# Kernel tuning notes

Measured on AMD Instinct MI355X. Metric: run time of the kernel, lower is better.

The kernel has to match this reference:

```python
import jax, jax.numpy as jnp
import numpy as np

B, T, L, C = 8, 512, 2048, 256

def setup_inputs() -> dict:
    key = jax.random.key(0)
    ks = jax.random.split(key, 8)
    # center/boundary positions in mel-frame units, a <= b
    e = jax.random.uniform(ks[0], (B, T), jnp.float32) * L
    a = jax.random.uniform(ks[1], (B, T), jnp.float32) * L
    w = jax.random.uniform(ks[2], (B, T), jnp.float32) * 20.0
    b = jnp.minimum(a + w, float(L))
    x_h = jax.random.normal(ks[3], (B, C, T), jnp.float32)
    text_mask = jnp.ones((B, T), dtype=bool)
    mel_mask = jnp.ones((B, L), dtype=jnp.float32)
    sigma = jnp.ones((2,), jnp.float32) * 0.1
    w_hidden = jax.random.normal(ks[4], (2 * C, C), jnp.float32) / np.sqrt(C)
    b_hidden = jnp.zeros((2 * C,), jnp.float32)
    w_out = jax.random.normal(ks[5], (C, 2 * C), jnp.float32) / np.sqrt(2 * C)
    b_out = jnp.zeros((C,), jnp.float32)
    return {"e": e, "a": a, "b": b, "x_h": x_h, "text_mask": text_mask,
            "mel_mask": mel_mask, "sigma": sigma, "w_hidden": w_hidden,
            "b_hidden": b_hidden, "w_out": w_out, "b_out": b_out}

def reference(e, a, b, x_h, text_mask, mel_mask, sigma, w_hidden, b_hidden, w_out, b_out):
    length = mel_mask.shape[-1]
    q = jnp.arange(length, dtype=e.dtype)[None, :] * mel_mask          # [B, L]
    qe = q[:, :, None]                                                 # [B, L, 1]
    energies_e = -((qe - e[:, None, :]) ** 2)                          # [B, L, T]
    energies_boundary = -((jnp.abs(qe - a[:, None, :]) + jnp.abs(qe - b[:, None, :])
                           - (b[:, None, :] - a[:, None, :])) ** 2)    # [B, L, T]
    energies_all = jnp.stack([energies_e, energies_boundary], axis=1)  # [B, 2, L, T]
    real_sigma = jnp.clip(sigma, 1e-6, 3.0)
    energies = energies_all * real_sigma[None, :, None, None]
    energies = jnp.where(text_mask[:, None, None, :], energies, -jnp.inf)
    attns = jax.nn.softmax(energies, axis=-1)                          # [B, 2, L, T]
    # 1x1 conv == channel matmul
    h = jnp.einsum('oc,bct->bot', w_hidden, x_h) + b_hidden[None, :, None]  # [B, 2C, T]
    Bh = h.shape[0]
    h = h.reshape(Bh, 2, C, T).transpose(0, 1, 3, 2)                   # [B, 2, T, C]
    out = jnp.matmul(attns, h)                                         # [B, 2, L, C]
    out = out.transpose(0, 1, 3, 2).reshape(Bh, 2 * C, length)         # [B, 2C, L]
    out = jnp.einsum('oc,bct->bot', w_out, out) + b_out[None, :, None] # [B, C, L]
    return (out, attns, real_sigma)
```

## Files before the change

### kernel.cpp

```cpp
#include <hip/hip_runtime.h>
#include <math.h>

#define B_ 8
#define T_ 512
#define L_ 2048
#define C_ 256

typedef short s16x8 __attribute__((ext_vector_type(8)));
typedef short s16x4 __attribute__((ext_vector_type(4)));
typedef float f32x4 __attribute__((ext_vector_type(4)));

static __device__ __forceinline__ short f2bf(float f) {
  unsigned int u = __float_as_uint(f);
  unsigned int r = u + 0x7FFFu + ((u >> 16) & 1u);
  return (short)(r >> 16);
}

__global__ __launch_bounds__(256) void k_fold(const float* __restrict__ wout,
                                              const float* __restrict__ whid,
                                              const float* __restrict__ bhid,
                                              unsigned short* __restrict__ W2bf,
                                              float* __restrict__ bias2) {
  int blk = blockIdx.x;
  int tid = threadIdx.x;
  if (blk < 512) {
    int s  = blk >> 8;
    int o  = ((blk >> 4) & 15) * 16 + (tid >> 4);
    int c2 = (blk & 15) * 16 + (tid & 15);
    const float* wo = wout + (size_t)o * 512 + s * 256;
    const float* wh = whid + (size_t)(s * 256) * 256 + c2;
    float a0 = 0.f, a1 = 0.f, a2 = 0.f, a3 = 0.f;
    for (int c = 0; c < 256; c += 4) {
      a0 += wo[c]     * wh[(size_t)c * 256];
      a1 += wo[c + 1] * wh[(size_t)(c + 1) * 256];
      a2 += wo[c + 2] * wh[(size_t)(c + 2) * 256];
      a3 += wo[c + 3] * wh[(size_t)(c + 3) * 256];
    }
    W2bf[((size_t)s * 256 + o) * 256 + c2] = (unsigned short)f2bf((a0 + a1) + (a2 + a3));
  } else {
    int s = blk - 512;
    int o = tid;
    const float* wo = wout + (size_t)o * 512 + s * 256;
    const float* bh = bhid + s * 256;
    float ab = 0.f;
    for (int c = 0; c < 256; ++c) ab += wo[c] * bh[c];
    bias2[s * 256 + o] = ab;
  }
}

__global__ __launch_bounds__(256) void k_hp(const float* __restrict__ xh,
                                            const unsigned short* __restrict__ W2bf,
                                            unsigned short* __restrict__ hpB) {
  __shared__ __align__(16) char lds[24576];
  char* As = lds;
  char* Bs = lds + 8192;
  int blk = blockIdx.x;
  int b  = blk >> 5;
  int m0 = ((blk >> 2) & 7) * 64;
  int n0 = (blk & 3) * 128;
  int tid = threadIdx.x;
  int wid = tid >> 6, lane = tid & 63;
  int ln15 = lane & 15, kg = lane >> 4;
  int tg = tid & 31, cg = tid >> 5;

  f32x4 acc[4][2];
#pragma unroll
  for (int mt = 0; mt < 4; ++mt)
#pragma unroll
    for (int nt = 0; nt < 2; ++nt) acc[mt][nt] = {0.f, 0.f, 0.f, 0.f};

  for (int k0 = 0; k0 < 256; k0 += 64) {
#pragma unroll
    for (int it = 0; it < 2; ++it) {
      int gi = it * 256 + tid;
      int r = gi >> 3, j = gi & 7;
      const unsigned short* src = W2bf + (size_t)(m0 + r) * 256 + k0 + ((j ^ (r & 7)) * 8);
      char* dst = As + (size_t)(it * 256 + wid * 64) * 16;
      __builtin_amdgcn_global_load_lds((const __attribute__((address_space(1))) void*)src,
                                       (__attribute__((address_space(3))) void*)dst, 16, 0, 0);
    }
    {
      float4 v[8];
#pragma unroll
      for (int cc = 0; cc < 8; ++cc)
        v[cc] = *(const float4*)&xh[((size_t)b * 256 + k0 + cg * 8 + cc) * 512 + n0 + tg * 4];
#pragma unroll
      for (int tt = 0; tt < 4; ++tt) {
        int trow = tg * 4 + tt;
        s16x8 w = {f2bf(v[0][tt]), f2bf(v[1][tt]), f2bf(v[2][tt]), f2bf(v[3][tt]),
                   f2bf(v[4][tt]), f2bf(v[5][tt]), f2bf(v[6][tt]), f2bf(v[7][tt])};
        *(s16x8*)(Bs + trow * 128 + ((cg ^ (trow & 7)) << 4)) = w;
      }
    }
    __syncthreads();
#pragma unroll
    for (int kk = 0; kk < 2; ++kk) {
      int sl = kk * 4 + kg;
      s16x8 af[4], bfr[2];
#pragma unroll
      for (int mt = 0; mt < 4; ++mt) {
        int r = mt * 16 + ln15;
        af[mt] = *(const s16x8*)(As + r * 128 + ((sl ^ (r & 7)) << 4));
      }
#pragma unroll
      for (int nt = 0; nt < 2; ++nt) {
        int r = wid * 32 + nt * 16 + ln15;
        bfr[nt] = *(const s16x8*)(Bs + r * 128 + ((sl ^ (r & 7)) << 4));
      }
#pragma unroll
      for (int mt = 0; mt < 4; ++mt)
#pragma unroll
        for (int nt = 0; nt < 2; ++nt)
          acc[mt][nt] = __builtin_amdgcn_mfma_f32_16x16x32_bf16(af[mt], bfr[nt], acc[mt][nt], 0, 0, 0);
    }
    __syncthreads();
  }
#pragma unroll
  for (int mt = 0; mt < 4; ++mt)
#pragma unroll
    for (int nt = 0; nt < 2; ++nt) {
      int n = n0 + wid * 32 + nt * 16 + ln15;
#pragma unroll
      for (int e = 0; e < 4; ++e) {
        int m = m0 + mt * 16 + kg * 4 + e;
        hpB[((size_t)b * 512 + m) * 512 + n] = (unsigned short)f2bf(acc[mt][nt][e]);
      }
    }
}

__global__ __launch_bounds__(512) void k_attnout(const float* __restrict__ pe,
                                                 const float* __restrict__ pa,
                                                 const float* __restrict__ pb,
                                                 const float* __restrict__ mel,
                                                 const float* __restrict__ sigma,
                                                 const float* __restrict__ bias2,
                                                 const float* __restrict__ bout,
                                                 const unsigned short* __restrict__ hpB,
                                                 float* __restrict__ outAttn,
                                                 float* __restrict__ outSigma,
                                                 float* __restrict__ out) {
  __shared__ __align__(16) char lds[73728];
  char* Bs0 = lds;
  char* As0 = lds + 65536;
  float* prm  = (float*)lds;
  float* stat = (float*)(lds + 6144);
  float* mval = (float*)(lds + 8192);
  float* idv  = (float*)(lds + 8448);

  int blk = blockIdx.x;
  int b  = blk & 7;
  int l0 = (blk >> 3) << 5;
  int tid = threadIdx.x;
  int wid = tid >> 6, lane = tid & 63;
  int ln15 = lane & 15, kg = lane >> 4;

  prm[tid]        = pe[b * 512 + tid];
  prm[512 + tid]  = pa[b * 512 + tid];
  prm[1024 + tid] = pb[b * 512 + tid];
  float sig0 = fminf(fmaxf(sigma[0], 1e-6f), 3.0f);
  float sig1 = fminf(fmaxf(sigma[1], 1e-6f), 3.0f);
  if (blk == 0 && tid < 2) outSigma[tid] = tid ? sig1 : sig0;
  __syncthreads();

  int pl = tid & 31, grp = tid >> 5;
  int s1 = grp & 1, et = grp >> 1;
  float qv1 = (float)(l0 + pl) * mel[(size_t)b * 2048 + l0 + pl];
  const float4* e4 = (const float4*)(prm + et * 64);
  const float4* a4 = (const float4*)(prm + 512 + et * 64);
  const float4* b4 = (const float4*)(prm + 1024 + et * 64);
  float pm = -INFINITY;
  if (s1 == 0) {
    for (int t4 = 0; t4 < 16; ++t4) {
      float4 ev = e4[t4];
#pragma unroll
      for (int j = 0; j < 4; ++j) {
        float de = qv1 - ev[j];
        pm = fmaxf(pm, -(de * de) * sig0);
      }
    }
  } else {
    for (int t4 = 0; t4 < 16; ++t4) {
      float4 av = a4[t4], bv = b4[t4];
#pragma unroll
      for (int j = 0; j < 4; ++j) {
        float d1 = fabsf(qv1 - av[j]) + fabsf(qv1 - bv[j]) - (bv[j] - av[j]);
        pm = fmaxf(pm, -(d1 * d1) * sig1);
      }
    }
  }
  stat[grp * 32 + pl] = pm;
  __syncthreads();
  if (tid < 64) {
    int s = tid >> 5, l = tid & 31;
    float m = stat[s * 32 + l];
#pragma unroll
    for (int g = 1; g < 8; ++g) m = fmaxf(m, stat[(g * 2 + s) * 32 + l]);
    mval[s * 32 + l] = m;
  }
  __syncthreads();
  float mm = mval[s1 * 32 + pl];
  float psum = 0.f;
  if (s1 == 0) {
    for (int t4 = 0; t4 < 16; ++t4) {
      float4 ev = e4[t4];
#pragma unroll
      for (int j = 0; j < 4; ++j) {
        float de = qv1 - ev[j];
        psum += __expf(fmaf(de * de, -sig0, -mm));
      }
    }
  } else {
    for (int t4 = 0; t4 < 16; ++t4) {
      float4 av = a4[t4], bv = b4[t4];
#pragma unroll
      for (int j = 0; j < 4; ++j) {
        float d1 = fabsf(qv1 - av[j]) + fabsf(qv1 - bv[j]) - (bv[j] - av[j]);
        psum += __expf(fmaf(d1 * d1, -sig1, -mm));
      }
    }
  }
  __syncthreads();
  stat[grp * 32 + pl] = psum;
  __syncthreads();
  if (tid < 64) {
    int s = tid >> 5, l = tid & 31;
    float sum = stat[s * 32 + l];
#pragma unroll
    for (int g = 1; g < 8; ++g) sum += stat[(g * 2 + s) * 32 + l];
    idv[s * 32 + l] = 1.0f / sum;
  }
  __syncthreads();

  {
    int row = tid >> 4, ts16 = tid & 15;
    float qv2 = (float)(l0 + row) * mel[(size_t)b * 2048 + l0 + row];
#pragma unroll
    for (int s = 0; s < 2; ++s) {
      float mm2 = mval[s * 32 + row];
      float iv2 = idv[s * 32 + row];
      float nmm = -mm2;
      float* ap = outAttn + ((size_t)(b * 2 + s) * 2048 + l0 + row) * 512;
#pragma unroll
      for (int j4 = 0; j4 < 8; ++j4) {
        int tb2 = j4 * 64 + ts16 * 4;
        f32x4 v;
        if (s == 0) {
          float4 ev = *(const float4*)(prm + tb2);
#pragma unroll
          for (int j = 0; j < 4; ++j) {
            float de = qv2 - ev[j];
            v[j] = __expf(fmaf(de * de, -sig0, nmm)) * iv2;
          }
        } else {
          float4 av = *(const float4*)(prm + 512 + tb2);
          float4 bv = *(const float4*)(prm + 1024 + tb2);
#pragma unroll
          for (int j = 0; j < 4; ++j) {
            float d1 = fabsf(qv2 - av[j]) + fabsf(qv2 - bv[j]) - (bv[j] - av[j]);
            v[j] = __expf(fmaf(d1 * d1, -sig1, nmm)) * iv2;
          }
        }
        *(f32x4*)(ap + tb2) = v;
      }
    }
  }
  asm volatile("s_waitcnt vmcnt(0)" ::: "memory");
  __builtin_amdgcn_sched_barrier(0);
  __syncthreads();

  int ar = tid >> 4, aj = tid & 15;

  f32x4 acc[2][2];
#pragma unroll
  for (int nt = 0; nt < 2; ++nt) {
    int o = wid * 32 + nt * 16 + ln15;
    float bv = bout[o] + bias2[o] + bias2[256 + o];
#pragma unroll
    for (int mt = 0; mt < 2; ++mt) acc[mt][nt] = {bv, bv, bv, bv};
  }

#define ISSUE_A(PH, AV)                                                                    \
  {                                                                                        \
    int s_ = (PH) & 1, t0_ = ((PH) >> 1) * 64;                                             \
    const float* ap = outAttn + ((size_t)(b * 2 + s_) * 2048 + l0 + ar) * 512 + t0_ + aj * 4;\
    AV = *(const f32x4*)ap;                                                                \
  }
#define ISSUE_B(PH)                                                                        \
  {                                                                                        \
    int s_ = (PH) & 1, t0_ = ((PH) >> 1) * 64;                                             \
    size_t hbase = ((size_t)(b * 2 + s_) * 256) * 512 + t0_;                               \
    char* dstbase = Bs0 + ((PH) & 1) * 32768;                                              \
    _Pragma("unroll")                                                                      \
    for (int it = 0; it < 4; ++it) {                                                       \
      int gi = it * 512 + tid;                                                             \
      int r = gi >> 3, j = gi & 7;                                                         \
      const unsigned short* src = hpB + hbase + (size_t)r * 512 + ((j ^ (r & 7)) * 8);     \
      char* dst = dstbase + (size_t)(it * 512 + wid * 64) * 16;                            \
      __builtin_amdgcn_global_load_lds((const __attribute__((address_space(1))) void*)src, \
                                       (__attribute__((address_space(3))) void*)dst,       \
                                       16, 0, 0);                                          \
    }                                                                                      \
  }
#define WRITE_A(PH, AV)                                                                    \
  {                                                                                        \
    char* Asb = As0 + ((PH) & 1) * 4096;                                                   \
    s16x4 pk = {f2bf(AV[0]), f2bf(AV[1]), f2bf(AV[2]), f2bf(AV[3])};                       \
    int slot8 = aj >> 1;                                                                   \
    *(s16x4*)(Asb + ar * 128 + ((slot8 ^ (ar & 7)) << 4) + ((aj & 1) << 3)) = pk;          \
  }

  {
    f32x4 av;
    ISSUE_A(0, av)
    ISSUE_B(0)
    WRITE_A(0, av)
    asm volatile("s_waitcnt lgkmcnt(0)" ::: "memory");
    asm volatile("s_waitcnt vmcnt(0)" ::: "memory");
    __builtin_amdgcn_sched_barrier(0);
    __builtin_amdgcn_s_barrier();
    __builtin_amdgcn_sched_barrier(0);
  }

  for (int p = 0; p < 16; ++p) {
    f32x4 av;
    if (p < 15) {
      ISSUE_A(p + 1, av)
      ISSUE_B(p + 1)
    }
    __builtin_amdgcn_sched_barrier(0);
    if (p < 15) asm volatile("s_waitcnt vmcnt(5)" ::: "memory");
    else        asm volatile("s_waitcnt vmcnt(0)" ::: "memory");
    __builtin_amdgcn_sched_barrier(0);
    {
      char* Asb = As0 + (p & 1) * 4096;
      char* Bsb = Bs0 + (p & 1) * 32768;
      __builtin_amdgcn_s_setprio(1);
#pragma unroll
      for (int kk = 0; kk < 2; ++kk) {
        int sl = kk * 4 + kg;
        s16x8 af[2], bq[2];
#pragma unroll
        for (int mt = 0; mt < 2; ++mt) {
          int r = mt * 16 + ln15;
          af[mt] = *(const s16x8*)(Asb + r * 128 + ((sl ^ (r & 7)) << 4));
        }
#pragma unroll
        for (int nt = 0; nt < 2; ++nt) {
          int r = wid * 32 + nt * 16 + ln15;
          bq[nt] = *(const s16x8*)(Bsb + r * 128 + ((sl ^ (r & 7)) << 4));
        }
#pragma unroll
        for (int mt = 0; mt < 2; ++mt)
#pragma unroll
          for (int nt = 0; nt < 2; ++nt)
            acc[mt][nt] = __builtin_amdgcn_mfma_f32_16x16x32_bf16(af[mt], bq[nt], acc[mt][nt], 0, 0, 0);
      }
      __builtin_amdgcn_s_setprio(0);
    }
    __builtin_amdgcn_sched_barrier(0);
    if (p < 15) {
      WRITE_A(p + 1, av)
      asm volatile("s_waitcnt lgkmcnt(0)" ::: "memory");
      __builtin_amdgcn_sched_barrier(0);
      __builtin_amdgcn_s_barrier();
      __builtin_amdgcn_sched_barrier(0);
    }
  }
#undef ISSUE_A
#undef ISSUE_B
#undef WRITE_A

#pragma unroll
  for (int nt = 0; nt < 2; ++nt) {
    int o = wid * 32 + nt * 16 + ln15;
    float* orow = out + ((size_t)b * 256 + o) * 2048 + l0 + kg * 4;
#pragma unroll
    for (int mt = 0; mt < 2; ++mt) {
      __builtin_nontemporal_store(acc[mt][nt], (f32x4*)(orow + mt * 16));
    }
  }
}

extern "C" void kernel_launch(void* const* d_in, const int* in_sizes, int n_in,
                              void* d_out, int out_size, void* d_ws, size_t ws_size,
                              hipStream_t stream) {
  (void)in_sizes; (void)n_in; (void)out_size; (void)ws_size;
  const float* e     = (const float*)d_in[0];
  const float* a     = (const float*)d_in[1];
  const float* bnd   = (const float*)d_in[2];
  const float* xh    = (const float*)d_in[3];
  const float* mel   = (const float*)d_in[5];
  const float* sigma = (const float*)d_in[6];
  const float* whid  = (const float*)d_in[7];
  const float* bhid  = (const float*)d_in[8];
  const float* wout  = (const float*)d_in[9];
  const float* bout  = (const float*)d_in[10];

  float* out      = (float*)d_out;
  float* outAttn  = out + (size_t)B_ * C_ * L_;
  float* outSigma = outAttn + (size_t)B_ * 2 * L_ * T_;

  unsigned short* W2bf = (unsigned short*)d_ws;
  float* bias2 = (float*)((char*)d_ws + 262144);
  unsigned short* hpB  = (unsigned short*)((char*)d_ws + 264192);

  hipLaunchKernelGGL(k_fold, dim3(514), dim3(256), 0, stream, wout, whid, bhid, W2bf, bias2);
  hipLaunchKernelGGL(k_hp,   dim3(256), dim3(256), 0, stream, xh, W2bf, hpB);
  hipLaunchKernelGGL(k_attnout, dim3(512), dim3(512), 0, stream,
                     e, a, bnd, mel, sigma, bias2, bout, hpB, outAttn, outSigma, out);
}
```

Measured before the change: 63.78 us.

## Fuse attention-probability generation into the GEMM loop instead of re-reading outAttn

Attention probabilities are now computed per K-phase inside the main MFMA loop. Each value is written to outAttn and packed to bf16 into LDS directly, so the separate write-all-then-reload-from-global pass is gone. The K tile shrinks from 64 to 32, which halves LDS use and may allow more resident blocks. The cost is twice as many loop iterations and barriers, plus a full vmcnt(0) wait every phase, so the B-tile prefetch no longer overlaps with the MFMAs.

```diff
diff --git a/kernel.cpp b/kernel.cpp
--- a/kernel.cpp
+++ b/kernel.cpp
@@ -8,7 +8,9 @@
 
 typedef short s16x8 __attribute__((ext_vector_type(8)));
 typedef short s16x4 __attribute__((ext_vector_type(4)));
+typedef short s16x2 __attribute__((ext_vector_type(2)));
 typedef float f32x4 __attribute__((ext_vector_type(4)));
+typedef float f32x2 __attribute__((ext_vector_type(2)));
 
 static __device__ __forceinline__ short f2bf(float f) {
   unsigned int u = __float_as_uint(f);
@@ -139,13 +141,13 @@
                                                  float* __restrict__ outAttn,
                                                  float* __restrict__ outSigma,
                                                  float* __restrict__ out) {
-  __shared__ __align__(16) char lds[73728];
-  char* Bs0 = lds;
-  char* As0 = lds + 65536;
-  float* prm  = (float*)lds;
-  float* stat = (float*)(lds + 6144);
-  float* mval = (float*)(lds + 8192);
-  float* idv  = (float*)(lds + 8448);
+  __shared__ __align__(16) char lds[45568];
+  char*  Bs0  = lds;
+  char*  As0  = lds + 32768;
+  float* prm  = (float*)(lds + 36864);
+  float* stat = (float*)(lds + 43008);
+  float* mval = (float*)(lds + 45056);
+  float* idv  = (float*)(lds + 45312);
 
   int blk = blockIdx.x;
   int b  = blk & 7;
@@ -231,44 +233,10 @@
   }
   __syncthreads();
 
-  {
-    int row = tid >> 4, ts16 = tid & 15;
-    float qv2 = (float)(l0 + row) * mel[(size_t)b * 2048 + l0 + row];
-#pragma unroll
-    for (int s = 0; s < 2; ++s) {
-      float mm2 = mval[s * 32 + row];
-      float iv2 = idv[s * 32 + row];
-      float nmm = -mm2;
-      float* ap = outAttn + ((size_t)(b * 2 + s) * 2048 + l0 + row) * 512;
-#pragma unroll
-      for (int j4 = 0; j4 < 8; ++j4) {
-        int tb2 = j4 * 64 + ts16 * 4;
-        f32x4 v;
-        if (s == 0) {
-          float4 ev = *(const float4*)(prm + tb2);
-#pragma unroll
-          for (int j = 0; j < 4; ++j) {
-            float de = qv2 - ev[j];
-            v[j] = __expf(fmaf(de * de, -sig0, nmm)) * iv2;
-          }
-        } else {
-          float4 av = *(const float4*)(prm + 512 + tb2);
-          float4 bv = *(const float4*)(prm + 1024 + tb2);
-#pragma unroll
-          for (int j = 0; j < 4; ++j) {
-            float d1 = fabsf(qv2 - av[j]) + fabsf(qv2 - bv[j]) - (bv[j] - av[j]);
-            v[j] = __expf(fmaf(d1 * d1, -sig1, nmm)) * iv2;
-          }
-        }
-        *(f32x4*)(ap + tb2) = v;
-      }
-    }
-  }
-  asm volatile("s_waitcnt vmcnt(0)" ::: "memory");
-  __builtin_amdgcn_sched_barrier(0);
-  __syncthreads();
-
-  int ar = tid >> 4, aj = tid & 15;
+  int row = tid >> 4, ts = tid & 15;
+  float qv2 = (float)(l0 + row) * mel[(size_t)b * 2048 + l0 + row];
+  float mm0 = mval[row],      iv0 = idv[row];
+  float mm1 = mval[32 + row], iv1 = idv[32 + row];
 
   f32x4 acc[2][2];
 #pragma unroll
@@ -279,41 +247,56 @@
     for (int mt = 0; mt < 2; ++mt) acc[mt][nt] = {bv, bv, bv, bv};
   }
 
-#define ISSUE_A(PH, AV)                                                                    \
+#define P_PHASE(PH, PK)                                                                    \
   {                                                                                        \
-    int s_ = (PH) & 1, t0_ = ((PH) >> 1) * 64;                                             \
-    const float* ap = outAttn + ((size_t)(b * 2 + s_) * 2048 + l0 + ar) * 512 + t0_ + aj * 4;\
-    AV = *(const f32x4*)ap;                                                                \
+    int s_ = (PH) & 1, t0_ = ((PH) >> 1) * 32;                                             \
+    int tw = t0_ + ts * 2;                                                                 \
+    float p0, p1;                                                                          \
+    if (s_ == 0) {                                                                         \
+      float e0 = prm[tw], e1 = prm[tw + 1];                                                \
+      float d0 = qv2 - e0, d1 = qv2 - e1;                                                  \
+      p0 = __expf(fmaf(d0 * d0, -sig0, -mm0)) * iv0;                                       \
+      p1 = __expf(fmaf(d1 * d1, -sig0, -mm0)) * iv0;                                       \
+    } else {                                                                               \
+      float a0 = prm[512 + tw], a1 = prm[512 + tw + 1];                                    \
+      float b0 = prm[1024 + tw], b1 = prm[1024 + tw + 1];                                  \
+      float d0 = fabsf(qv2 - a0) + fabsf(qv2 - b0) - (b0 - a0);                            \
+      float d1 = fabsf(qv2 - a1) + fabsf(qv2 - b1) - (b1 - a1);                            \
+      p0 = __expf(fmaf(d0 * d0, -sig1, -mm1)) * iv1;                                       \
+      p1 = __expf(fmaf(d1 * d1, -sig1, -mm1)) * iv1;                                       \
+    }                                                                                      \
+    f32x2 v = {p0, p1};                                                                    \
+    *(f32x2*)(outAttn + ((size_t)(b * 2 + s_) * 2048 + l0 + row) * 512 + tw) = v;          \
+    PK = (s16x2){f2bf(p0), f2bf(p1)};                                                      \
+  }
+#define WRITE_AS(PH, PK)                                                                   \
+  {                                                                                        \
+    char* Asb = As0 + ((PH) & 1) * 2048;                                                   \
+    int sl = (ts >> 2) ^ ((row >> 1) & 3);                                                 \
+    *(s16x2*)(Asb + row * 64 + (sl << 4) + ((ts & 3) << 2)) = PK;                          \
   }
 #define ISSUE_B(PH)                                                                        \
   {                                                                                        \
-    int s_ = (PH) & 1, t0_ = ((PH) >> 1) * 64;                                             \
+    int s_ = (PH) & 1, t0_ = ((PH) >> 1) * 32;                                             \
     size_t hbase = ((size_t)(b * 2 + s_) * 256) * 512 + t0_;                               \
-    char* dstbase = Bs0 + ((PH) & 1) * 32768;                                              \
+    char* dstbase = Bs0 + ((PH) & 1) * 16384;                                              \
     _Pragma("unroll")                                                                      \
-    for (int it = 0; it < 4; ++it) {                                                       \
+    for (int it = 0; it < 2; ++it) {                                                       \
       int gi = it * 512 + tid;                                                             \
-      int r = gi >> 3, j = gi & 7;                                                         \
-      const unsigned short* src = hpB + hbase + (size_t)r * 512 + ((j ^ (r & 7)) * 8);     \
+      int r = gi >> 2, jd = gi & 3;                                                        \
+      const unsigned short* src = hpB + hbase + (size_t)r * 512 + ((jd ^ ((r >> 1) & 3)) * 8);\
       char* dst = dstbase + (size_t)(it * 512 + wid * 64) * 16;                            \
       __builtin_amdgcn_global_load_lds((const __attribute__((address_space(1))) void*)src, \
                                        (__attribute__((address_space(3))) void*)dst,       \
                                        16, 0, 0);                                          \
     }                                                                                      \
   }
-#define WRITE_A(PH, AV)                                                                    \
-  {                                                                                        \
-    char* Asb = As0 + ((PH) & 1) * 4096;                                                   \
-    s16x4 pk = {f2bf(AV[0]), f2bf(AV[1]), f2bf(AV[2]), f2bf(AV[3])};                       \
-    int slot8 = aj >> 1;                                                                   \
-    *(s16x4*)(Asb + ar * 128 + ((slot8 ^ (ar & 7)) << 4) + ((aj & 1) << 3)) = pk;          \
-  }
 
   {
-    f32x4 av;
-    ISSUE_A(0, av)
+    s16x2 pk;
+    P_PHASE(0, pk)
+    WRITE_AS(0, pk)
     ISSUE_B(0)
-    WRITE_A(0, av)
     asm volatile("s_waitcnt lgkmcnt(0)" ::: "memory");
     asm volatile("s_waitcnt vmcnt(0)" ::: "memory");
     __builtin_amdgcn_sched_barrier(0);
@@ -321,54 +304,48 @@
     __builtin_amdgcn_sched_barrier(0);
   }
 
-  for (int p = 0; p < 16; ++p) {
-    f32x4 av;
-    if (p < 15) {
-      ISSUE_A(p + 1, av)
+  for (int p = 0; p < 32; ++p) {
+    {
+      char* Asb = As0 + (p & 1) * 2048;
+      char* Bsb = Bs0 + (p & 1) * 16384;
+      __builtin_amdgcn_s_setprio(1);
+      s16x8 af[2], bq[2];
+#pragma unroll
+      for (int mt = 0; mt < 2; ++mt) {
+        int r = mt * 16 + ln15;
+        af[mt] = *(const s16x8*)(Asb + r * 64 + ((kg ^ ((r >> 1) & 3)) << 4));
+      }
+#pragma unroll
+      for (int nt = 0; nt < 2; ++nt) {
+        int r = wid * 32 + nt * 16 + ln15;
+        bq[nt] = *(const s16x8*)(Bsb + r * 64 + ((kg ^ ((r >> 1) & 3)) << 4));
+      }
+#pragma unroll
+      for (int mt = 0; mt < 2; ++mt)
+#pragma unroll
+        for (int nt = 0; nt < 2; ++nt)
+          acc[mt][nt] = __builtin_amdgcn_mfma_f32_16x16x32_bf16(af[mt], bq[nt], acc[mt][nt], 0, 0, 0);
+      __builtin_amdgcn_s_setprio(0);
+    }
+    __builtin_amdgcn_sched_barrier(0);
+    __builtin_amdgcn_s_barrier();
+    __builtin_amdgcn_sched_barrier(0);
+    if (p < 31) {
+      s16x2 pk;
+      P_PHASE(p + 1, pk)
+      WRITE_AS(p + 1, pk)
       ISSUE_B(p + 1)
-    }
-    __builtin_amdgcn_sched_barrier(0);
-    if (p < 15) asm volatile("s_waitcnt vmcnt(5)" ::: "memory");
-    else        asm volatile("s_waitcnt vmcnt(0)" ::: "memory");
-    __builtin_amdgcn_sched_barrier(0);
-    {
-      char* Asb = As0 + (p & 1) * 4096;
-      char* Bsb = Bs0 + (p & 1) * 32768;
-      __builtin_amdgcn_s_setprio(1);
-#pragma unroll
-      for (int kk = 0; kk < 2; ++kk) {
-        int sl = kk * 4 + kg;
-        s16x8 af[2], bq[2];
-#pragma unroll
-        for (int mt = 0; mt < 2; ++mt) {
-          int r = mt * 16 + ln15;
-          af[mt] = *(const s16x8*)(Asb + r * 128 + ((sl ^ (r & 7)) << 4));
-        }
-#pragma unroll
-        for (int nt = 0; nt < 2; ++nt) {
-          int r = wid * 32 + nt * 16 + ln15;
-          bq[nt] = *(const s16x8*)(Bsb + r * 128 + ((sl ^ (r & 7)) << 4));
-        }
-#pragma unroll
-        for (int mt = 0; mt < 2; ++mt)
-#pragma unroll
-          for (int nt = 0; nt < 2; ++nt)
-            acc[mt][nt] = __builtin_amdgcn_mfma_f32_16x16x32_bf16(af[mt], bq[nt], acc[mt][nt], 0, 0, 0);
-      }
-      __builtin_amdgcn_s_setprio(0);
-    }
-    __builtin_amdgcn_sched_barrier(0);
-    if (p < 15) {
-      WRITE_A(p + 1, av)
+      __builtin_amdgcn_sched_barrier(0);
       asm volatile("s_waitcnt lgkmcnt(0)" ::: "memory");
+      asm volatile("s_waitcnt vmcnt(0)" ::: "memory");
       __builtin_amdgcn_sched_barrier(0);
       __builtin_amdgcn_s_barrier();
       __builtin_amdgcn_sched_barrier(0);
     }
   }
-#undef ISSUE_A
+#undef P_PHASE
+#undef WRITE_AS
 #undef ISSUE_B
-#undef WRITE_A
 
 #pragma unroll
   for (int nt = 0; nt < 2; ++nt) {
```

Result: slower. 69.70 us (+9.3%).

## Sort token positions and restrict attention matmul to a non-negligible rank window

Applied to the files above, without the earlier changes.

A new prep kernel bitonic-sorts each batch's centre and boundary positions, records each token's rank, the max width, and a per-frame start-rank table. The projection kernel writes its bf16 output permuted into sorted-rank order. The fused attention kernel then uses sigma and the row max to bound the band of tokens whose softmax weight exceeds about e^-27.6. It runs the MFMA matmul only over those rank tiles, recomputing the probabilities there instead of re-reading the full attention matrix from global memory. In exchange it adds a launch, scattered strided stores in the projection kernel, and a single-buffered loop without load/compute overlap, and it drops terms below the cutoff.

```diff
diff --git a/kernel.cpp b/kernel.cpp
--- a/kernel.cpp
+++ b/kernel.cpp
@@ -14,6 +14,63 @@
   unsigned int u = __float_as_uint(f);
   unsigned int r = u + 0x7FFFu + ((u >> 16) & 1u);
   return (short)(r >> 16);
+}
+
+__global__ __launch_bounds__(512) void k_prep(const float* __restrict__ e,
+                                              const float* __restrict__ a,
+                                              const float* __restrict__ bnd,
+                                              float* __restrict__ sortK1,
+                                              float* __restrict__ sortK2,
+                                              int* __restrict__ startRank,
+                                              float* __restrict__ wmax,
+                                              int* __restrict__ rankOf) {
+  __shared__ float k1s[512];
+  __shared__ float k2s[512];
+  __shared__ int   ids[512];
+  __shared__ float red[512];
+  int bs = blockIdx.x;
+  int b = bs >> 1, s = bs & 1;
+  int tid = threadIdx.x;
+  float k1, k2;
+  if (s == 0) { k1 = e[b * 512 + tid]; k2 = k1; }
+  else        { k1 = a[b * 512 + tid]; k2 = bnd[b * 512 + tid]; }
+  k1s[tid] = k1; k2s[tid] = k2; ids[tid] = tid;
+  red[tid] = k2 - k1;
+  __syncthreads();
+  for (int off = 256; off > 0; off >>= 1) {
+    if (tid < off) red[tid] = fmaxf(red[tid], red[tid + off]);
+    __syncthreads();
+  }
+  if (tid == 0) wmax[bs] = red[0];
+  for (int k = 2; k <= 512; k <<= 1) {
+    for (int j = k >> 1; j > 0; j >>= 1) {
+      int ixj = tid ^ j;
+      if (ixj > tid) {
+        bool up = ((tid & k) == 0);
+        float x1 = k1s[tid], y1 = k1s[ixj];
+        if ((x1 > y1) == up) {
+          k1s[tid] = y1; k1s[ixj] = x1;
+          float x2 = k2s[tid]; k2s[tid] = k2s[ixj]; k2s[ixj] = x2;
+          int xi = ids[tid]; ids[tid] = ids[ixj]; ids[ixj] = xi;
+        }
+      }
+      __syncthreads();
+    }
+  }
+  sortK1[bs * 576 + tid] = k1s[tid];
+  sortK2[bs * 576 + tid] = k2s[tid];
+  rankOf[bs * 512 + ids[tid]] = tid;
+  if (tid < 64) {
+    sortK1[bs * 576 + 512 + tid] = 1e9f;
+    sortK2[bs * 576 + 512 + tid] = 1e9f;
+  }
+  __syncthreads();
+  for (int p = tid; p < 2049; p += 512) {
+    float pf = (float)p;
+    int lo = 0, hi = 512;
+    while (lo < hi) { int mid = (lo + hi) >> 1; if (k1s[mid] < pf) lo = mid + 1; else hi = mid; }
+    startRank[bs * 2049 + p] = lo;
+  }
 }
 
 __global__ __launch_bounds__(256) void k_fold(const float* __restrict__ wout,
@@ -50,7 +107,8 @@
 
 __global__ __launch_bounds__(256) void k_hp(const float* __restrict__ xh,
                                             const unsigned short* __restrict__ W2bf,
-                                            unsigned short* __restrict__ hpB) {
+                                            const int* __restrict__ rankOf,
+                                            unsigned short* __restrict__ hpS) {
   __shared__ __align__(16) char lds[24576];
   char* As = lds;
   char* Bs = lds + 8192;
@@ -115,17 +173,21 @@
     }
     __syncthreads();
   }
-#pragma unroll
-  for (int mt = 0; mt < 4; ++mt)
-#pragma unroll
-    for (int nt = 0; nt < 2; ++nt) {
-      int n = n0 + wid * 32 + nt * 16 + ln15;
-#pragma unroll
-      for (int e = 0; e < 4; ++e) {
-        int m = m0 + mt * 16 + kg * 4 + e;
-        hpB[((size_t)b * 512 + m) * 512 + n] = (unsigned short)f2bf(acc[mt][nt][e]);
-      }
-    }
+  int s_hp = m0 >> 8;
+  int bs2 = b * 2 + s_hp;
+#pragma unroll
+  for (int nt = 0; nt < 2; ++nt) {
+    int n = n0 + wid * 32 + nt * 16 + ln15;
+    int rank = rankOf[bs2 * 512 + n];
+#pragma unroll
+    for (int mt = 0; mt < 4; ++mt)
+#pragma unroll
+      for (int e2 = 0; e2 < 4; ++e2) {
+        int m = m0 + mt * 16 + kg * 4 + e2;
+        int o = m & 255;
+        hpS[((size_t)bs2 * 256 + o) * 576 + rank] = (unsigned short)f2bf(acc[mt][nt][e2]);
+      }
+  }
 }
 
 __global__ __launch_bounds__(512) void k_attnout(const float* __restrict__ pe,
@@ -135,17 +197,23 @@
                                                  const float* __restrict__ sigma,
                                                  const float* __restrict__ bias2,
                                                  const float* __restrict__ bout,
-                                                 const unsigned short* __restrict__ hpB,
+                                                 const unsigned short* __restrict__ hpS,
+                                                 const float* __restrict__ sortK1,
+                                                 const float* __restrict__ sortK2,
+                                                 const int* __restrict__ startRank,
+                                                 const float* __restrict__ wmax,
                                                  float* __restrict__ outAttn,
                                                  float* __restrict__ outSigma,
                                                  float* __restrict__ out) {
-  __shared__ __align__(16) char lds[73728];
-  char* Bs0 = lds;
-  char* As0 = lds + 65536;
-  float* prm  = (float*)lds;
-  float* stat = (float*)(lds + 6144);
-  float* mval = (float*)(lds + 8192);
-  float* idv  = (float*)(lds + 8448);
+  __shared__ __align__(16) char lds[43808];
+  char*  Bs   = lds;
+  char*  As   = lds + 32768;
+  float* prm  = (float*)(lds + 36864);
+  float* mval = (float*)(lds + 43008);
+  float* idv  = (float*)(lds + 43264);
+  float* red2 = (float*)(lds + 43520);
+  int*   bw   = (int*)(lds + 43776);
+  float* stat = (float*)lds;
 
   int blk = blockIdx.x;
   int b  = blk & 7;
@@ -231,44 +299,58 @@
   }
   __syncthreads();
 
-  {
-    int row = tid >> 4, ts16 = tid & 15;
-    float qv2 = (float)(l0 + row) * mel[(size_t)b * 2048 + l0 + row];
-#pragma unroll
-    for (int s = 0; s < 2; ++s) {
-      float mm2 = mval[s * 32 + row];
-      float iv2 = idv[s * 32 + row];
-      float nmm = -mm2;
-      float* ap = outAttn + ((size_t)(b * 2 + s) * 2048 + l0 + row) * 512;
-#pragma unroll
-      for (int j4 = 0; j4 < 8; ++j4) {
-        int tb2 = j4 * 64 + ts16 * 4;
-        f32x4 v;
-        if (s == 0) {
-          float4 ev = *(const float4*)(prm + tb2);
-#pragma unroll
-          for (int j = 0; j < 4; ++j) {
-            float de = qv2 - ev[j];
-            v[j] = __expf(fmaf(de * de, -sig0, nmm)) * iv2;
-          }
-        } else {
-          float4 av = *(const float4*)(prm + 512 + tb2);
-          float4 bv = *(const float4*)(prm + 1024 + tb2);
-#pragma unroll
-          for (int j = 0; j < 4; ++j) {
-            float d1 = fabsf(qv2 - av[j]) + fabsf(qv2 - bv[j]) - (bv[j] - av[j]);
-            v[j] = __expf(fmaf(d1 * d1, -sig1, nmm)) * iv2;
-          }
-        }
-        *(f32x4*)(ap + tb2) = v;
-      }
-    }
-  }
-  asm volatile("s_waitcnt vmcnt(0)" ::: "memory");
-  __builtin_amdgcn_sched_barrier(0);
-  __syncthreads();
-
-  int ar = tid >> 4, aj = tid & 15;
+  if (tid < 64) {
+    int s = tid >> 5;
+    float sg = s ? sig1 : sig0;
+    red2[tid] = sqrtf(fmaxf(27.6f - mval[tid], 0.f) / sg);
+  }
+  __syncthreads();
+  if (tid < 2) {
+    float mx = 0.f;
+    for (int i = 0; i < 32; ++i) mx = fmaxf(mx, red2[tid * 32 + i]);
+    float lo = (float)l0 - mx - (tid ? wmax[b * 2 + 1] : 0.f);
+    float hi = (float)(l0 + 31) + mx;
+    int pl_ = min(max((int)floorf(lo), 0), 2048);
+    int ph_ = min(max((int)ceilf(hi) + 1, 0), 2048);
+    int r0 = startRank[(b * 2 + tid) * 2049 + pl_];
+    int r1 = startRank[(b * 2 + tid) * 2049 + ph_];
+    int r0a = r0 & ~7;
+    bw[tid * 2]     = r0a;
+    bw[tid * 2 + 1] = max(0, (r1 - r0a + 63) >> 6);
+  }
+
+  int row = tid >> 4, ts = tid & 15;
+  float qv2 = (float)(l0 + row) * mel[(size_t)b * 2048 + l0 + row];
+  float mm0 = mval[row],      iv0 = idv[row];
+  float mm1 = mval[32 + row], iv1 = idv[32 + row];
+
+  for (int ph = 0; ph < 16; ++ph) {
+    int s_ = ph & 1, t0_ = (ph >> 1) * 64;
+    int tw = t0_ + ts * 4;
+    float P0, P1, P2, P3;
+    if (s_ == 0) {
+      float4 ev = *(const float4*)(prm + tw);
+      float d0 = qv2 - ev[0], d1 = qv2 - ev[1], d2 = qv2 - ev[2], d3 = qv2 - ev[3];
+      P0 = __expf(fmaf(d0 * d0, -sig0, -mm0)) * iv0;
+      P1 = __expf(fmaf(d1 * d1, -sig0, -mm0)) * iv0;
+      P2 = __expf(fmaf(d2 * d2, -sig0, -mm0)) * iv0;
+      P3 = __expf(fmaf(d3 * d3, -sig0, -mm0)) * iv0;
+    } else {
+      float4 av = *(const float4*)(prm + 512 + tw);
+      float4 bv = *(const float4*)(prm + 1024 + tw);
+      float d0 = fabsf(qv2 - av[0]) + fabsf(qv2 - bv[0]) - (bv[0] - av[0]);
+      float d1 = fabsf(qv2 - av[1]) + fabsf(qv2 - bv[1]) - (bv[1] - av[1]);
+      float d2 = fabsf(qv2 - av[2]) + fabsf(qv2 - bv[2]) - (bv[2] - av[2]);
+      float d3 = fabsf(qv2 - av[3]) + fabsf(qv2 - bv[3]) - (bv[3] - av[3]);
+      P0 = __expf(fmaf(d0 * d0, -sig1, -mm1)) * iv1;
+      P1 = __expf(fmaf(d1 * d1, -sig1, -mm1)) * iv1;
+      P2 = __expf(fmaf(d2 * d2, -sig1, -mm1)) * iv1;
+      P3 = __expf(fmaf(d3 * d3, -sig1, -mm1)) * iv1;
+    }
+    f32x4 v = {P0, P1, P2, P3};
+    *(f32x4*)(outAttn + ((size_t)(b * 2 + s_) * 2048 + l0 + row) * 512 + tw) = v;
+  }
+  __syncthreads();
 
   f32x4 acc[2][2];
 #pragma unroll
@@ -279,62 +361,53 @@
     for (int mt = 0; mt < 2; ++mt) acc[mt][nt] = {bv, bv, bv, bv};
   }
 
-#define ISSUE_A(PH, AV)                                                                    \
-  {                                                                                        \
-    int s_ = (PH) & 1, t0_ = ((PH) >> 1) * 64;                                             \
-    const float* ap = outAttn + ((size_t)(b * 2 + s_) * 2048 + l0 + ar) * 512 + t0_ + aj * 4;\
-    AV = *(const f32x4*)ap;                                                                \
-  }
-#define ISSUE_B(PH)                                                                        \
-  {                                                                                        \
-    int s_ = (PH) & 1, t0_ = ((PH) >> 1) * 64;                                             \
-    size_t hbase = ((size_t)(b * 2 + s_) * 256) * 512 + t0_;                               \
-    char* dstbase = Bs0 + ((PH) & 1) * 32768;                                              \
-    _Pragma("unroll")                                                                      \
-    for (int it = 0; it < 4; ++it) {                                                       \
-      int gi = it * 512 + tid;                                                             \
-      int r = gi >> 3, j = gi & 7;                                                         \
-      const unsigned short* src = hpB + hbase + (size_t)r * 512 + ((j ^ (r & 7)) * 8);     \
-      char* dst = dstbase + (size_t)(it * 512 + wid * 64) * 16;                            \
-      __builtin_amdgcn_global_load_lds((const __attribute__((address_space(1))) void*)src, \
-                                       (__attribute__((address_space(3))) void*)dst,       \
-                                       16, 0, 0);                                          \
-    }                                                                                      \
-  }
-#define WRITE_A(PH, AV)                                                                    \
-  {                                                                                        \
-    char* Asb = As0 + ((PH) & 1) * 4096;                                                   \
-    s16x4 pk = {f2bf(AV[0]), f2bf(AV[1]), f2bf(AV[2]), f2bf(AV[3])};                       \
-    int slot8 = aj >> 1;                                                                   \
-    *(s16x4*)(Asb + ar * 128 + ((slot8 ^ (ar & 7)) << 4) + ((aj & 1) << 3)) = pk;          \
-  }
-
-  {
-    f32x4 av;
-    ISSUE_A(0, av)
-    ISSUE_B(0)
-    WRITE_A(0, av)
-    asm volatile("s_waitcnt lgkmcnt(0)" ::: "memory");
-    asm volatile("s_waitcnt vmcnt(0)" ::: "memory");
-    __builtin_amdgcn_sched_barrier(0);
-    __builtin_amdgcn_s_barrier();
-    __builtin_amdgcn_sched_barrier(0);
-  }
-
-  for (int p = 0; p < 16; ++p) {
-    f32x4 av;
-    if (p < 15) {
-      ISSUE_A(p + 1, av)
-      ISSUE_B(p + 1)
-    }
-    __builtin_amdgcn_sched_barrier(0);
-    if (p < 15) asm volatile("s_waitcnt vmcnt(5)" ::: "memory");
-    else        asm volatile("s_waitcnt vmcnt(0)" ::: "memory");
-    __builtin_amdgcn_sched_barrier(0);
-    {
-      char* Asb = As0 + (p & 1) * 4096;
-      char* Bsb = Bs0 + (p & 1) * 32768;
-      __builtin_amdgcn_s_setprio(1);
+  for (int s = 0; s < 2; ++s) {
+    int r0a = bw[s * 2], KT = bw[s * 2 + 1];
+    float mmS = s ? mm1 : mm0, ivS = s ? iv1 : iv0, sgS = s ? sig1 : sig0;
+    const float* K1 = sortK1 + (b * 2 + s) * 576;
+    const float* K2 = sortK2 + (b * 2 + s) * 576;
+    size_t hbase = ((size_t)(b * 2 + s) * 256) * 576;
+    for (int t = 0; t < KT; ++t) {
+      int rb = r0a + t * 64;
+      {
+        int rk = rb + ts * 4;
+        float4 v1 = *(const float4*)(K1 + rk);
+        float P0, P1, P2, P3;
+        if (s == 0) {
+          float d0 = qv2 - v1.x, d1 = qv2 - v1.y, d2 = qv2 - v1.z, d3 = qv2 - v1.w;
+          P0 = __expf(fmaf(d0 * d0, -sgS, -mmS)) * ivS;
+          P1 = __expf(fmaf(d1 * d1, -sgS, -mmS)) * ivS;
+          P2 = __expf(fmaf(d2 * d2, -sgS, -mmS)) * ivS;
+          P3 = __expf(fmaf(d3 * d3, -sgS, -mmS)) * ivS;
+        } else {
+          float4 v2 = *(const float4*)(K2 + rk);
+          float d0 = fabsf(qv2 - v1.x) + fabsf(qv2 - v2.x) - (v2.x - v1.x);
+          float d1 = fabsf(qv2 - v1.y) + fabsf(qv2 - v2.y) - (v2.y - v1.y);
+          float d2 = fabsf(qv2 - v1.z) + fabsf(qv2 - v2.z) - (v2.z - v1.z);
+          float d3 = fabsf(qv2 - v1.w) + fabsf(qv2 - v2.w) - (v2.w - v1.w);
+          P0 = __expf(fmaf(d0 * d0, -sgS, -mmS)) * ivS;
+          P1 = __expf(fmaf(d1 * d1, -sgS, -mmS)) * ivS;
+          P2 = __expf(fmaf(d2 * d2, -sgS, -mmS)) * ivS;
+          P3 = __expf(fmaf(d3 * d3, -sgS, -mmS)) * ivS;
+        }
+        s16x4 pk = {f2bf(P0), f2bf(P1), f2bf(P2), f2bf(P3)};
+        int sl16 = ts >> 1;
+        *(s16x4*)(As + row * 128 + ((sl16 ^ (row & 7)) << 4) + ((ts & 1) << 3)) = pk;
+      }
+#pragma unroll
+      for (int it = 0; it < 4; ++it) {
+        int gi = it * 512 + tid;
+        int r = gi >> 3, jd = gi & 7;
+        const unsigned short* src = hpS + hbase + (size_t)r * 576 + rb + ((jd ^ (r & 7)) * 8);
+        char* dst = Bs + (size_t)(it * 512 + wid * 64) * 16;
+        __builtin_amdgcn_global_load_lds((const __attribute__((address_space(1))) void*)src,
+                                         (__attribute__((address_space(3))) void*)dst, 16, 0, 0);
+      }
+      asm volatile("s_waitcnt lgkmcnt(0)" ::: "memory");
+      asm volatile("s_waitcnt vmcnt(0)" ::: "memory");
+      __builtin_amdgcn_sched_barrier(0);
+      __builtin_amdgcn_s_barrier();
+      __builtin_amdgcn_sched_barrier(0);
 #pragma unroll
       for (int kk = 0; kk < 2; ++kk) {
         int sl = kk * 4 + kg;
@@ -342,12 +415,12 @@
 #pragma unroll
         for (int mt = 0; mt < 2; ++mt) {
           int r = mt * 16 + ln15;
-          af[mt] = *(const s16x8*)(Asb + r * 128 + ((sl ^ (r & 7)) << 4));
+          af[mt] = *(const s16x8*)(As + r * 128 + ((sl ^ (r & 7)) << 4));
         }
 #pragma unroll
         for (int nt = 0; nt < 2; ++nt) {
           int r = wid * 32 + nt * 16 + ln15;
-          bq[nt] = *(const s16x8*)(Bsb + r * 128 + ((sl ^ (r & 7)) << 4));
+          bq[nt] = *(const s16x8*)(Bs + r * 128 + ((sl ^ (r & 7)) << 4));
         }
 #pragma unroll
         for (int mt = 0; mt < 2; ++mt)
@@ -355,20 +428,11 @@
           for (int nt = 0; nt < 2; ++nt)
             acc[mt][nt] = __builtin_amdgcn_mfma_f32_16x16x32_bf16(af[mt], bq[nt], acc[mt][nt], 0, 0, 0);
       }
-      __builtin_amdgcn_s_setprio(0);
-    }
-    __builtin_amdgcn_sched_barrier(0);
-    if (p < 15) {
-      WRITE_A(p + 1, av)
-      asm volatile("s_waitcnt lgkmcnt(0)" ::: "memory");
       __builtin_amdgcn_sched_barrier(0);
       __builtin_amdgcn_s_barrier();
       __builtin_amdgcn_sched_barrier(0);
     }
   }
-#undef ISSUE_A
-#undef ISSUE_B
-#undef WRITE_A
 
 #pragma unroll
   for (int nt = 0; nt < 2; ++nt) {
@@ -400,12 +464,21 @@
   float* outAttn  = out + (size_t)B_ * C_ * L_;
   float* outSigma = outAttn + (size_t)B_ * 2 * L_ * T_;
 
-  unsigned short* W2bf = (unsigned short*)d_ws;
-  float* bias2 = (float*)((char*)d_ws + 262144);
-  unsigned short* hpB  = (unsigned short*)((char*)d_ws + 264192);
-
+  char* ws = (char*)d_ws;
+  unsigned short* W2bf   = (unsigned short*)ws;
+  float*          bias2  = (float*)(ws + 262144);
+  float*          sortK1 = (float*)(ws + 264192);
+  float*          sortK2 = (float*)(ws + 301056);
+  int*            startR = (int*)(ws + 337920);
+  float*          wmax   = (float*)(ws + 469056);
+  int*            rankOf = (int*)(ws + 469120);
+  unsigned short* hpS    = (unsigned short*)(ws + 501888);
+
+  hipLaunchKernelGGL(k_prep, dim3(16),  dim3(512), 0, stream, e, a, bnd,
+                     sortK1, sortK2, startR, wmax, rankOf);
   hipLaunchKernelGGL(k_fold, dim3(514), dim3(256), 0, stream, wout, whid, bhid, W2bf, bias2);
-  hipLaunchKernelGGL(k_hp,   dim3(256), dim3(256), 0, stream, xh, W2bf, hpB);
+  hipLaunchKernelGGL(k_hp,   dim3(256), dim3(256), 0, stream, xh, W2bf, rankOf, hpS);
   hipLaunchKernelGGL(k_attnout, dim3(512), dim3(512), 0, stream,
-                     e, a, bnd, mel, sigma, bias2, bout, hpB, outAttn, outSigma, out);
-}
+                     e, a, bnd, mel, sigma, bias2, bout, hpS, sortK1, sortK2, startR, wmax,
+                     outAttn, outSigma, out);
+}
```

Measured after the change: 74.21 us. 16.3% more time.
